# Optimization experiments

Hardware: AMD Instinct MI355X
Metric: run time of the kernel (lower is better)

## Reference

```python
import jax, jax.numpy as jnp
import numpy as np
from jax import lax

ALPHA = 0.5       # voxel vs structure weighting
BETA = 0.5        # split vs merge weighting
THRESHOLD = 0.0   # logit threshold for binarizing predictions
N_ITERS = 48      # label-propagation + pointer-jumping rounds (effective reach ~2^N)


def _shift(x, axis, s):
    """Shift x by s along axis, zero-filling the boundary (labels are >= 0)."""
    pads = [(0, 0)] * x.ndim
    pads[axis] = (max(s, 0), max(-s, 0))
    xp = jnp.pad(x, pads)
    idx = [slice(None)] * x.ndim
    idx[axis] = slice(max(-s, 0), max(-s, 0) + x.shape[axis])
    return xp[tuple(idx)]


def label_ccl(mask):
    """Connected-component labeling of a 3D boolean mask with 6-connectivity
    (scipy.ndimage.label default structure). Each component ends up holding the
    max linear index (+1) of its voxels; background is 0. Uses max-propagation
    over the 6-neighborhood plus pointer jumping for fast convergence."""
    size = mask.size
    ids = jnp.arange(1, size + 1, dtype=jnp.int32).reshape(mask.shape)
    lbl0 = jnp.where(mask, ids, 0)

    def body(_, lbl):
        m = lbl
        for ax in range(3):
            for s in (1, -1):
                m = jnp.maximum(m, _shift(lbl, ax, s))
        m = jnp.where(mask, m, 0)
        # pointer jumping: look up the label stored at the voxel my label points to
        hop = m.ravel()[jnp.maximum(m - 1, 0)]
        return jnp.where(mask, jnp.maximum(m, hop), 0)

    return lax.fori_loop(0, N_ITERS, body, lbl0)


def detect_critical(labels, other_fg):
    """Mark every connected component of `labels` that is not fully covered by
    the other segmentation's foreground (i.e., contains at least one mistake);
    the whole component is flagged as a structure-level (critical) error."""
    size = labels.size
    err = (labels > 0) & (~other_fg)
    has_err = jax.ops.segment_max(
        err.ravel().astype(jnp.int32), labels.ravel(), num_segments=size + 1
    )
    return ((has_err[labels] > 0) & (labels > 0)).astype(jnp.float32)


def setup_inputs() -> dict:
    key = jax.random.key(0)
    k1, k2 = jax.random.split(key)
    preds = jax.random.normal(k1, (2, 2, 128, 128, 128), dtype=jnp.float32)
    targets = jax.random.randint(k2, (2, 1, 128, 128, 128), 0, 2, dtype=jnp.int32)
    return {"preds": preds, "targets": targets}


def reference(preds, targets):
    # per-voxel robust cross entropy (reduction='none') over the 2-class channel dim
    tgt = targets[:, 0].astype(jnp.int32)                      # (B, D, H, W)
    logp = jax.nn.log_softmax(preds, axis=1)                   # (B, 2, D, H, W)
    loss = -jnp.take_along_axis(logp, tgt[:, None], axis=1)[:, 0]  # (B, D, H, W)

    # binarize and label both segmentations (apply_nonlin=None -> raw logits)
    pred_fg = preds[:, 1] > THRESHOLD
    tgt_fg = tgt > 0
    pred_lbl = jax.vmap(label_ccl)(pred_fg)
    tgt_lbl = jax.vmap(label_ccl)(tgt_fg)

    # critical_type=-1 (pred vs target components) scaled by beta,
    # critical_type=+1 (target vs pred components) scaled by (1 - beta)
    m_neg = jax.vmap(detect_critical)(tgt_lbl, pred_fg)
    m_pos = jax.vmap(detect_critical)(pred_lbl, tgt_fg)
    crit = BETA * m_neg + (1.0 - BETA) * m_pos

    # blend voxel-level and structure-level loss, then mean over the batch
    loss = (1.0 - ALPHA) * loss + ALPHA * crit * loss
    return loss.mean()
```

## Files before the change

### kernel.cpp

```cpp
#include <hip/hip_runtime.h>
#include <math.h>

#define VOL   (128 * 128 * 128)
#define NB    2
#define TOTAL (NB * VOL)

#define INVP   0x7FFFFFFFu
#define FLAGB  0x80000000u
#define TAGB   0x40000000u
#define GIDM   0x3FFFFFFFu
#define IDXM   0x7FFFFFFFu
#define LINV   0xFFFFFFFFu

#define TPV            (8 * 8 * 8)
#define FACES_PER_DIR  (7 * 8 * 8)
#define FACES_PER_VOL  (3 * FACES_PER_DIR)
#define NFACES         (NB * FACES_PER_VOL)

__device__ __forceinline__ unsigned find_root(unsigned* P, unsigned i) {
    while (true) {
        unsigned p = P[i] & IDXM;
        if (p == i) return i;
        unsigned gp = P[p] & IDXM;
        if (gp != p) atomicMin(&P[i], gp);
        i = gp;
    }
}

__device__ __forceinline__ void unite(unsigned* P, unsigned a, unsigned b) {
    a = find_root(P, a);
    b = find_root(P, b);
    while (a != b) {
        if (b > a) { unsigned t = a; a = b; b = t; }
        unsigned old = atomicMin(&P[a], b);
        if (old == a) return;
        a = find_root(P, old & IDXM);
        b = find_root(P, b);
    }
}

__device__ __forceinline__ unsigned lfind(unsigned* L, unsigned i) {
    while (true) {
        unsigned p = L[i];
        if (p == i) return i;
        unsigned gp = L[p];
        if (gp != p) atomicMin(&L[i], gp);
        i = gp;
    }
}

__device__ __forceinline__ void lunite(unsigned* L, unsigned a, unsigned b) {
    a = lfind(L, a);
    b = lfind(L, b);
    while (a != b) {
        if (b > a) { unsigned t = a; a = b; b = t; }
        unsigned old = atomicMin(&L[a], b);
        if (old == a) return;
        a = lfind(L, old);
        b = lfind(L, b);
    }
}


__global__ void k_zero(unsigned* __restrict__ cnts) {
    if (threadIdx.x < 4) cnts[threadIdx.x] = 0;
}

__global__ void k_local(const float* __restrict__ preds,
                        const int* __restrict__ tgt,
                        unsigned* __restrict__ Pp,
                        unsigned* __restrict__ Pt,
                        unsigned* __restrict__ list,
                        unsigned* __restrict__ cnts,
                        unsigned cap) {
    __shared__ unsigned lpp[4096], lpt[4096];
    __shared__ unsigned perr[128], terr[128];
    __shared__ unsigned s_scan[256];
    __shared__ unsigned s_gbase;
    unsigned tile = blockIdx.x;
    unsigned b  = tile >> 9;
    unsigned tz = (tile >> 6) & 7, ty = (tile >> 3) & 7, tx = tile & 7;
    unsigned base_v = tz * (16 * 16384) + ty * (16 * 128) + tx * 16;
    unsigned base_g = b * VOL + base_v;

    if (threadIdx.x < 128) { perr[threadIdx.x] = 0; terr[threadIdx.x] = 0; }
    for (int base = threadIdx.x * 4; base < 4096; base += 1024) {
        unsigned lx = base & 15, ly = (base >> 4) & 15, lz = base >> 8;
        unsigned voli = base_v + lz * 16384 + ly * 128 + lx;
        float4 p1 = *reinterpret_cast<const float4*>(
            preds + (size_t)(b * 2 + 1) * VOL + voli);
        int4  t4 = *reinterpret_cast<const int4*>(tgt + b * VOL + voli);
        uint4 vp, vt;
        vp.x = (p1.x > 0.0f) ? (unsigned)(base + 0) : LINV;
        vp.y = (p1.y > 0.0f) ? (unsigned)(base + 1) : LINV;
        vp.z = (p1.z > 0.0f) ? (unsigned)(base + 2) : LINV;
        vp.w = (p1.w > 0.0f) ? (unsigned)(base + 3) : LINV;
        vt.x = (t4.x > 0) ? (unsigned)(base + 0) : LINV;
        vt.y = (t4.y > 0) ? (unsigned)(base + 1) : LINV;
        vt.z = (t4.z > 0) ? (unsigned)(base + 2) : LINV;
        vt.w = (t4.w > 0) ? (unsigned)(base + 3) : LINV;
        *reinterpret_cast<uint4*>(&lpp[base]) = vp;
        *reinterpret_cast<uint4*>(&lpt[base]) = vt;
    }
    __syncthreads();

    for (int l = threadIdx.x; l < 4096; l += 256) {
        unsigned lx = l & 15, ly = (l >> 4) & 15, lz = l >> 8;
        if (lpp[l] != LINV) {
            if (lx < 15 && lpp[l + 1]   != LINV) lunite(lpp, l, l + 1);
            if (ly < 15 && lpp[l + 16]  != LINV) lunite(lpp, l, l + 16);
            if (lz < 15 && lpp[l + 256] != LINV) lunite(lpp, l, l + 256);
        }
        if (lpt[l] != LINV) {
            if (lx < 15 && lpt[l + 1]   != LINV) lunite(lpt, l, l + 1);
            if (ly < 15 && lpt[l + 16]  != LINV) lunite(lpt, l, l + 16);
            if (lz < 15 && lpt[l + 256] != LINV) lunite(lpt, l, l + 256);
        }
    }
    __syncthreads();

    for (int l = threadIdx.x; l < 4096; l += 256) {
        unsigned lx = l & 15, ly = (l >> 4) & 15, lz = l >> 8;
        unsigned g = base_g + lz * 16384 + ly * 128 + lx;
        bool pf = lpp[l] != LINV, tf = lpt[l] != LINV;
        if (pf) {
            unsigned r = lfind(lpp, l);
            Pp[g] = base_g + (r >> 8) * 16384 + ((r >> 4) & 15) * 128 + (r & 15);
            if (!tf) atomicOr(&perr[r >> 5], 1u << (r & 31));
        } else Pp[g] = INVP;
        if (tf) {
            unsigned r = lfind(lpt, l);
            Pt[g] = base_g + (r >> 8) * 16384 + ((r >> 4) & 15) * 128 + (r & 15);
            if (!pf) atomicOr(&terr[r >> 5], 1u << (r & 31));
        } else Pt[g] = INVP;
    }
    __syncthreads();

    unsigned myCnt = 0;
    for (int k = 0; k < 16; ++k) {
        int l = threadIdx.x + k * 256;
        myCnt += (lpp[l] == (unsigned)l) + (lpt[l] == (unsigned)l);
    }
    s_scan[threadIdx.x] = myCnt;
    __syncthreads();
    for (int off = 1; off < 256; off <<= 1) {
        unsigned v = (threadIdx.x >= (unsigned)off) ? s_scan[threadIdx.x - off] : 0u;
        __syncthreads();
        s_scan[threadIdx.x] += v;
        __syncthreads();
    }
    if (threadIdx.x == 255) s_gbase = atomicAdd(&cnts[0], s_scan[255]);
    unsigned mybase = s_scan[threadIdx.x] - myCnt;
    __syncthreads();
    unsigned idx = s_gbase + mybase;
    for (int k = 0; k < 16; ++k) {
        int l = threadIdx.x + k * 256;
        unsigned gid = base_g + (l >> 8) * 16384 + ((l >> 4) & 15) * 128 + (l & 15);
        if (lpp[l] == (unsigned)l) {
            if (idx < cap) {
                unsigned eb = (perr[l >> 5] >> (l & 31)) & 1u;
                list[idx] = gid | (eb ? FLAGB : 0u);
            }
            idx++;
        }
        if (lpt[l] == (unsigned)l) {
            if (idx < cap) {
                unsigned eb = (terr[l >> 5] >> (l & 31)) & 1u;
                list[idx] = gid | TAGB | (eb ? FLAGB : 0u);
            }
            idx++;
        }
    }
}

__global__ void k_bmerge(unsigned* __restrict__ Pp, unsigned* __restrict__ Pt) {
    unsigned fid = blockIdx.x;
    unsigned vol = fid / FACES_PER_VOL;
    unsigned r   = fid % FACES_PER_VOL;
    unsigned dir = r / FACES_PER_DIR;
    unsigned fr  = r % FACES_PER_DIR;
    unsigned b0 = fr % 7;
    unsigned t1 = (fr / 7) % 8;
    unsigned t2 = fr / 56;
    unsigned u = threadIdx.x & 15, v = threadIdx.x >> 4;
    unsigned lane = threadIdx.x & 63;

    unsigned x, y, z, step;
    if (dir == 0)      { x = b0 * 16 + 15; y = t1 * 16 + u; z = t2 * 16 + v; step = 1; }
    else if (dir == 1) { y = b0 * 16 + 15; x = t1 * 16 + u; z = t2 * 16 + v; step = 128; }
    else               { z = b0 * 16 + 15; x = t1 * 16 + u; y = t2 * 16 + v; step = 16384; }
    unsigned g = vol * VOL + z * 16384 + y * 128 + x;

    for (int arr = 0; arr < 2; ++arr) {
        unsigned* P = arr ? Pt : Pp;
        unsigned a = P[g];
        unsigned bb = P[g + step];
        bool need = (a != INVP) && (bb != INVP);
        bool leader = false;
        unsigned long long rem = __ballot(need);
        while (rem) {
            int src = __ffsll(rem) - 1;
            unsigned sa = __shfl(a, src), sb = __shfl(bb, src);
            if (need && a == sa && bb == sb) {
                leader = ((int)lane == src);
                need = false;
            }
            rem = __ballot(need);
        }
        if (leader) unite(P, a, bb);
    }
}

__global__ void k_rcompress(unsigned* __restrict__ Pp, unsigned* __restrict__ Pt,
                            const unsigned* __restrict__ list,
                            const unsigned* __restrict__ cnts, unsigned cap) {
    unsigned n = cnts[0] < cap ? cnts[0] : cap;
    for (unsigned i = blockIdx.x * blockDim.x + threadIdx.x; i < n;
         i += gridDim.x * blockDim.x) {
        unsigned e = list[i];
        unsigned* P = (e & TAGB) ? Pt : Pp;
        unsigned r = e & GIDM;
        unsigned rt = find_root(P, r);
        if (rt != r) atomicMin(&P[r], rt);
        if ((e & FLAGB) && !(P[rt] & FLAGB)) atomicOr(&P[rt], FLAGB);
    }
}

__global__ void k_rpull(unsigned* __restrict__ Pp, unsigned* __restrict__ Pt,
                        const unsigned* __restrict__ list,
                        const unsigned* __restrict__ cnts, unsigned cap) {
    unsigned n = cnts[0] < cap ? cnts[0] : cap;
    for (unsigned i = blockIdx.x * blockDim.x + threadIdx.x; i < n;
         i += gridDim.x * blockDim.x) {
        unsigned e = list[i];
        unsigned* P = (e & TAGB) ? Pt : Pp;
        unsigned r = e & GIDM;
        unsigned root = P[r] & IDXM;
        if ((P[root] & FLAGB) && !(P[r] & FLAGB)) atomicOr(&P[r], FLAGB);
    }
}

__global__ void k_loss(const float* __restrict__ preds,
                       const int* __restrict__ tgt,
                       const unsigned* __restrict__ Pp,
                       const unsigned* __restrict__ Pt,
                       float* __restrict__ partial) {
    float acc = 0.0f;
    for (unsigned g4 = (blockIdx.x * blockDim.x + threadIdx.x) * 4; g4 < TOTAL;
         g4 += gridDim.x * blockDim.x * 4) {
        unsigned b = g4 >> 21;
        unsigned i = g4 & (VOL - 1);
        float4 p0 = *reinterpret_cast<const float4*>(preds + (size_t)(b * 2 + 0) * VOL + i);
        float4 p1 = *reinterpret_cast<const float4*>(preds + (size_t)(b * 2 + 1) * VOL + i);
        int4  t4  = *reinterpret_cast<const int4*>(tgt + g4);
        uint4 vp4 = *reinterpret_cast<const uint4*>(Pp + g4);
        uint4 vt4 = *reinterpret_cast<const uint4*>(Pt + g4);
        float p0a[4] = {p0.x, p0.y, p0.z, p0.w};
        float p1a[4] = {p1.x, p1.y, p1.z, p1.w};
        int   ta[4]  = {t4.x, t4.y, t4.z, t4.w};
        unsigned vpa[4] = {vp4.x, vp4.y, vp4.z, vp4.w};
        unsigned vta[4] = {vt4.x, vt4.y, vt4.z, vt4.w};
        #pragma unroll
        for (int j = 0; j < 4; ++j) {
            float z  = (ta[j] > 0) ? (p0a[j] - p1a[j]) : (p1a[j] - p0a[j]);
            float ce = (z > 0.0f) ? (z + log1pf(expf(-z))) : log1pf(expf(z));
            float crit = 0.0f;
            if (vta[j] != INVP) {
                unsigned r = vta[j] & IDXM;
                if (Pt[r] & FLAGB) crit += 0.5f;
            }
            if (vpa[j] != INVP) {
                unsigned r = vpa[j] & IDXM;
                if (Pp[r] & FLAGB) crit += 0.5f;
            }
            acc += 0.5f * ce * (1.0f + crit);
        }
    }
    for (int off = 32; off > 0; off >>= 1) acc += __shfl_down(acc, off);
    __shared__ float s[4];
    int wid = threadIdx.x >> 6, lane = threadIdx.x & 63;
    if (lane == 0) s[wid] = acc;
    __syncthreads();
    if (threadIdx.x == 0) {
        float tacc = 0.0f;
        for (int w = 0; w < (int)(blockDim.x >> 6); ++w) tacc += s[w];
        partial[blockIdx.x] = tacc;
    }
}

__global__ void k_final(const float* __restrict__ partial, int n,
                        float* __restrict__ out) {
    double acc = 0.0;
    for (int i = threadIdx.x; i < n; i += blockDim.x) acc += (double)partial[i];
    for (int off = 32; off > 0; off >>= 1) acc += __shfl_down(acc, off);
    __shared__ double s[4];
    int wid = threadIdx.x >> 6, lane = threadIdx.x & 63;
    if (lane == 0) s[wid] = acc;
    __syncthreads();
    if (threadIdx.x == 0) {
        double t = 0.0;
        for (int w = 0; w < (int)(blockDim.x >> 6); ++w) t += s[w];
        out[0] = (float)(t / (double)TOTAL);
    }
}


extern "C" void kernel_launch(void* const* d_in, const int* in_sizes, int n_in,
                              void* d_out, int out_size, void* d_ws, size_t ws_size,
                              hipStream_t stream) {
    const float* preds   = (const float*)d_in[0];
    const int*   targets = (const int*)d_in[1];
    float*       out     = (float*)d_out;

    unsigned* Pp = (unsigned*)d_ws;
    unsigned* Pt = Pp + TOTAL;
    float* partial = (float*)(Pt + TOTAL);
    unsigned* cnts = (unsigned*)(partial + 2048);
    unsigned* list = cnts + 4;
    size_t used = (size_t)((char*)list - (char*)d_ws);
    size_t avail = ws_size > used ? ws_size - used : 0;
    size_t cap_sz = avail / 4;
    unsigned cap = cap_sz > 1048576 ? 1048576u : (unsigned)cap_sz;

    const int T = 256;
    const int NTILE = NB * TPV;
    k_zero     <<<1, 64, 0, stream>>>(cnts);
    k_local    <<<NTILE, T, 0, stream>>>(preds, targets, Pp, Pt, list, cnts, cap);
    k_bmerge   <<<NFACES, T, 0, stream>>>(Pp, Pt);
    k_rcompress<<<128, T, 0, stream>>>(Pp, Pt, list, cnts, cap);
    k_rpull    <<<128, T, 0, stream>>>(Pp, Pt, list, cnts, cap);

    const int RB = 2048;
    k_loss <<<RB, T, 0, stream>>>(preds, targets, Pp, Pt, partial);
    k_final<<<1, T, 0, stream>>>(partial, RB, out);
}
```

Baseline: 261.6 us.

## Process pred and target labels sequentially in one shared array with wave-shuffle scan

```diff
diff --git a/kernel.cpp b/kernel.cpp
--- a/kernel.cpp
+++ b/kernel.cpp
@@ -73,103 +73,105 @@
                         unsigned* __restrict__ list,
                         unsigned* __restrict__ cnts,
                         unsigned cap) {
-    __shared__ unsigned lpp[4096], lpt[4096];
-    __shared__ unsigned perr[128], terr[128];
-    __shared__ unsigned s_scan[256];
+    __shared__ unsigned lab[4096];
+    __shared__ unsigned fgP[128], fgT[128], errb[128];
+    __shared__ unsigned s_wtot[4];
     __shared__ unsigned s_gbase;
     unsigned tile = blockIdx.x;
     unsigned b  = tile >> 9;
     unsigned tz = (tile >> 6) & 7, ty = (tile >> 3) & 7, tx = tile & 7;
     unsigned base_v = tz * (16 * 16384) + ty * (16 * 128) + tx * 16;
     unsigned base_g = b * VOL + base_v;
-
-    if (threadIdx.x < 128) { perr[threadIdx.x] = 0; terr[threadIdx.x] = 0; }
+    unsigned lane = threadIdx.x & 63, wid = threadIdx.x >> 6;
+
+    if (threadIdx.x < 128) { fgP[threadIdx.x] = 0; fgT[threadIdx.x] = 0; }
+    __syncthreads();
     for (int base = threadIdx.x * 4; base < 4096; base += 1024) {
         unsigned lx = base & 15, ly = (base >> 4) & 15, lz = base >> 8;
         unsigned voli = base_v + lz * 16384 + ly * 128 + lx;
         float4 p1 = *reinterpret_cast<const float4*>(
             preds + (size_t)(b * 2 + 1) * VOL + voli);
         int4  t4 = *reinterpret_cast<const int4*>(tgt + b * VOL + voli);
-        uint4 vp, vt;
-        vp.x = (p1.x > 0.0f) ? (unsigned)(base + 0) : LINV;
-        vp.y = (p1.y > 0.0f) ? (unsigned)(base + 1) : LINV;
-        vp.z = (p1.z > 0.0f) ? (unsigned)(base + 2) : LINV;
-        vp.w = (p1.w > 0.0f) ? (unsigned)(base + 3) : LINV;
-        vt.x = (t4.x > 0) ? (unsigned)(base + 0) : LINV;
-        vt.y = (t4.y > 0) ? (unsigned)(base + 1) : LINV;
-        vt.z = (t4.z > 0) ? (unsigned)(base + 2) : LINV;
-        vt.w = (t4.w > 0) ? (unsigned)(base + 3) : LINV;
-        *reinterpret_cast<uint4*>(&lpp[base]) = vp;
-        *reinterpret_cast<uint4*>(&lpt[base]) = vt;
+        unsigned pm = ((p1.x > 0.0f) ? 1u : 0u) | ((p1.y > 0.0f) ? 2u : 0u) |
+                      ((p1.z > 0.0f) ? 4u : 0u) | ((p1.w > 0.0f) ? 8u : 0u);
+        unsigned tm = ((t4.x > 0) ? 1u : 0u) | ((t4.y > 0) ? 2u : 0u) |
+                      ((t4.z > 0) ? 4u : 0u) | ((t4.w > 0) ? 8u : 0u);
+        if (pm) atomicOr(&fgP[base >> 5], pm << (base & 31));
+        if (tm) atomicOr(&fgT[base >> 5], tm << (base & 31));
     }
     __syncthreads();
 
-    for (int l = threadIdx.x; l < 4096; l += 256) {
-        unsigned lx = l & 15, ly = (l >> 4) & 15, lz = l >> 8;
-        if (lpp[l] != LINV) {
-            if (lx < 15 && lpp[l + 1]   != LINV) lunite(lpp, l, l + 1);
-            if (ly < 15 && lpp[l + 16]  != LINV) lunite(lpp, l, l + 16);
-            if (lz < 15 && lpp[l + 256] != LINV) lunite(lpp, l, l + 256);
-        }
-        if (lpt[l] != LINV) {
-            if (lx < 15 && lpt[l + 1]   != LINV) lunite(lpt, l, l + 1);
-            if (ly < 15 && lpt[l + 16]  != LINV) lunite(lpt, l, l + 16);
-            if (lz < 15 && lpt[l + 256] != LINV) lunite(lpt, l, l + 256);
-        }
-    }
-    __syncthreads();
-
-    for (int l = threadIdx.x; l < 4096; l += 256) {
-        unsigned lx = l & 15, ly = (l >> 4) & 15, lz = l >> 8;
-        unsigned g = base_g + lz * 16384 + ly * 128 + lx;
-        bool pf = lpp[l] != LINV, tf = lpt[l] != LINV;
-        if (pf) {
-            unsigned r = lfind(lpp, l);
-            Pp[g] = base_g + (r >> 8) * 16384 + ((r >> 4) & 15) * 128 + (r & 15);
-            if (!tf) atomicOr(&perr[r >> 5], 1u << (r & 31));
-        } else Pp[g] = INVP;
-        if (tf) {
-            unsigned r = lfind(lpt, l);
-            Pt[g] = base_g + (r >> 8) * 16384 + ((r >> 4) & 15) * 128 + (r & 15);
-            if (!pf) atomicOr(&terr[r >> 5], 1u << (r & 31));
-        } else Pt[g] = INVP;
-    }
-    __syncthreads();
-
-    unsigned myCnt = 0;
-    for (int k = 0; k < 16; ++k) {
-        int l = threadIdx.x + k * 256;
-        myCnt += (lpp[l] == (unsigned)l) + (lpt[l] == (unsigned)l);
-    }
-    s_scan[threadIdx.x] = myCnt;
-    __syncthreads();
-    for (int off = 1; off < 256; off <<= 1) {
-        unsigned v = (threadIdx.x >= (unsigned)off) ? s_scan[threadIdx.x - off] : 0u;
-        __syncthreads();
-        s_scan[threadIdx.x] += v;
-        __syncthreads();
-    }
-    if (threadIdx.x == 255) s_gbase = atomicAdd(&cnts[0], s_scan[255]);
-    unsigned mybase = s_scan[threadIdx.x] - myCnt;
-    __syncthreads();
-    unsigned idx = s_gbase + mybase;
-    for (int k = 0; k < 16; ++k) {
-        int l = threadIdx.x + k * 256;
-        unsigned gid = base_g + (l >> 8) * 16384 + ((l >> 4) & 15) * 128 + (l & 15);
-        if (lpp[l] == (unsigned)l) {
-            if (idx < cap) {
-                unsigned eb = (perr[l >> 5] >> (l & 31)) & 1u;
-                list[idx] = gid | (eb ? FLAGB : 0u);
-            }
-            idx++;
-        }
-        if (lpt[l] == (unsigned)l) {
-            if (idx < cap) {
-                unsigned eb = (terr[l >> 5] >> (l & 31)) & 1u;
-                list[idx] = gid | TAGB | (eb ? FLAGB : 0u);
-            }
-            idx++;
-        }
+    for (int arr = 0; arr < 2; ++arr) {
+        unsigned* FG = arr ? fgT : fgP;
+        unsigned* OG = arr ? fgP : fgT;
+        unsigned* P  = arr ? Pt : Pp;
+        unsigned tag = arr ? TAGB : 0u;
+
+        for (int base = threadIdx.x * 4; base < 4096; base += 1024) {
+            unsigned w = FG[base >> 5] >> (base & 31);
+            uint4 v;
+            v.x = (w & 1u) ? (unsigned)(base + 0) : LINV;
+            v.y = (w & 2u) ? (unsigned)(base + 1) : LINV;
+            v.z = (w & 4u) ? (unsigned)(base + 2) : LINV;
+            v.w = (w & 8u) ? (unsigned)(base + 3) : LINV;
+            *reinterpret_cast<uint4*>(&lab[base]) = v;
+        }
+        if (threadIdx.x < 128) errb[threadIdx.x] = 0;
+        __syncthreads();
+
+        for (int l = threadIdx.x; l < 4096; l += 256) {
+            if (lab[l] != LINV) {
+                unsigned lx = l & 15, ly = (l >> 4) & 15, lz = l >> 8;
+                if (lx < 15 && lab[l + 1]   != LINV) lunite(lab, l, l + 1);
+                if (ly < 15 && lab[l + 16]  != LINV) lunite(lab, l, l + 16);
+                if (lz < 15 && lab[l + 256] != LINV) lunite(lab, l, l + 256);
+            }
+        }
+        __syncthreads();
+
+        for (int l = threadIdx.x; l < 4096; l += 256) {
+            unsigned lx = l & 15, ly = (l >> 4) & 15, lz = l >> 8;
+            unsigned g = base_g + lz * 16384 + ly * 128 + lx;
+            if (lab[l] != LINV) {
+                unsigned r = lfind(lab, l);
+                P[g] = base_g + (r >> 8) * 16384 + ((r >> 4) & 15) * 128 + (r & 15);
+                if (!((OG[l >> 5] >> (l & 31)) & 1u))
+                    atomicOr(&errb[r >> 5], 1u << (r & 31));
+            } else P[g] = INVP;
+        }
+        __syncthreads();
+
+        unsigned myCnt = 0;
+        for (int k = 0; k < 16; ++k) {
+            int l = threadIdx.x + k * 256;
+            myCnt += (lab[l] == (unsigned)l) ? 1u : 0u;
+        }
+        unsigned inc = myCnt;
+        for (int off = 1; off < 64; off <<= 1) {
+            unsigned n = __shfl_up(inc, off);
+            if (lane >= (unsigned)off) inc += n;
+        }
+        if (lane == 63) s_wtot[wid] = inc;
+        __syncthreads();
+        if (threadIdx.x == 0) {
+            unsigned tot = 0;
+            for (int w = 0; w < 4; ++w) { unsigned t = s_wtot[w]; s_wtot[w] = tot; tot += t; }
+            s_gbase = atomicAdd(&cnts[0], tot);
+        }
+        __syncthreads();
+        unsigned idx = s_gbase + s_wtot[wid] + inc - myCnt;
+        for (int k = 0; k < 16; ++k) {
+            int l = threadIdx.x + k * 256;
+            if (lab[l] == (unsigned)l) {
+                if (idx < cap) {
+                    unsigned gid = base_g + (l >> 8) * 16384 + ((l >> 4) & 15) * 128 + (l & 15);
+                    unsigned eb = (errb[l >> 5] >> (l & 31)) & 1u;
+                    list[idx] = gid | tag | (eb ? FLAGB : 0u);
+                }
+                idx++;
+            }
+        }
+        __syncthreads();
     }
 }
 
```

Result: slower. 288.7 us (+10.4%).
